# Performance work log

Hardware: AMD Instinct MI355X
Metric: run time of the kernel (lower is better)

Reference implementation:

```python
import jax, jax.numpy as jnp
import numpy as np
from jax import lax

D_MODEL = 768
N_LAYER = 4
D_STATE = 16
D_CONV = 4
EXPAND = 2
VOCAB = 32000
B = 1
L = 1024
D_INNER = D_MODEL * EXPAND
EPS = 1e-5


def setup_inputs() -> dict:
    key = jax.random.key(0)
    ks = jax.random.split(key, 8)
    s = 0.02
    A_row = jnp.log(jnp.arange(1, D_STATE + 1, dtype=jnp.float32))  # log(1..N)
    return {
        "idx": jax.random.randint(ks[0], (B, L), 0, VOCAB),
        "embed": jax.random.normal(ks[1], (VOCAB, D_MODEL), jnp.float32) * s,
        "norm_w": jnp.ones((N_LAYER, D_MODEL), jnp.float32),
        "W_in": jax.random.normal(ks[2], (N_LAYER, 2 * D_INNER, D_MODEL), jnp.float32) * s,
        "conv_w": jax.random.normal(ks[3], (N_LAYER, D_INNER, 1, D_CONV), jnp.float32) * s,
        "conv_b": jnp.zeros((N_LAYER, D_INNER), jnp.float32),
        "W_x": jax.random.normal(ks[4], (N_LAYER, 2 * D_STATE + 1, D_INNER), jnp.float32) * s,
        "dt_w": jax.random.normal(ks[5], (N_LAYER, D_INNER, 1), jnp.float32) * s,
        "dt_b": jnp.zeros((N_LAYER, D_INNER), jnp.float32),
        "A_log": jnp.tile(A_row, (N_LAYER, D_INNER, 1)),
        "Dp": jnp.ones((N_LAYER, D_INNER), jnp.float32),
        "out_w": jax.random.normal(ks[6], (N_LAYER, D_MODEL, D_INNER), jnp.float32) * s,
        "norm_f_w": jnp.ones((D_MODEL,), jnp.float32),
    }


def rmsnorm(x, w):
    return x / jnp.sqrt(jnp.mean(x * x, axis=-1, keepdims=True) + EPS) * w


def selective_scan(xc, W_x, dt_w, dt_b, A_log, Dp):
    # xc: [B, L, D_INNER]
    A = -jnp.exp(A_log)                               # [D, N]
    xp = xc @ W_x.T                                   # [B, L, 2N+1]
    dt_r = xp[..., :1]
    Bv = xp[..., 1:1 + D_STATE]                       # [B, L, N]
    Cv = xp[..., 1 + D_STATE:]                        # [B, L, N]
    dt = jax.nn.softplus(dt_r * dt_w[:, 0] + dt_b)    # [B, L, D]
    dA = jnp.exp(dt[..., None] * A)                   # [B, L, D, N]
    dBx = dt[..., None] * Bv[:, :, None, :] * xc[..., None]  # [B, L, D, N]

    def step(h, inp):
        dA_t, dBx_t, C_t = inp
        h = dA_t * h + dBx_t                          # [B, D, N]
        y = jnp.einsum('bdn,bn->bd', h, C_t)          # [B, D]
        return h, y

    h0 = jnp.zeros((xc.shape[0], D_INNER, D_STATE), xc.dtype)
    _, ys = lax.scan(step, h0, (dA.transpose(1, 0, 2, 3),
                                dBx.transpose(1, 0, 2, 3),
                                Cv.transpose(1, 0, 2)))
    return ys.transpose(1, 0, 2) + xc * Dp            # [B, L, D]


def mamba_block(x, W_in, conv_w, conv_b, W_x, dt_w, dt_b, A_log, Dp, out_w):
    xz = x @ W_in.T                                   # [B, L, 2*D_INNER]
    x_ssm, z = jnp.split(xz, 2, axis=-1)
    # depthwise causal conv1d (torch pads both sides then keeps first L == left pad only)
    xc = lax.conv_general_dilated(x_ssm.transpose(0, 2, 1), conv_w, (1,),
                                  [(D_CONV - 1, 0)],
                                  feature_group_count=D_INNER,
                                  dimension_numbers=('NCH', 'OIH', 'NCH'))
    xc = (xc + conv_b[None, :, None]).transpose(0, 2, 1)
    xc = jax.nn.silu(xc)
    y = selective_scan(xc, W_x, dt_w, dt_b, A_log, Dp)
    y = y * jax.nn.silu(z)
    return y @ out_w.T


def reference(idx, embed, norm_w, W_in, conv_w, conv_b, W_x, dt_w, dt_b, A_log, Dp, out_w, norm_f_w):
    x = embed[idx]  # dropout in eval mode == identity
    for i in range(N_LAYER):
        x = x + mamba_block(rmsnorm(x, norm_w[i]), W_in[i], conv_w[i], conv_b[i],
                            W_x[i], dt_w[i], dt_b[i], A_log[i], Dp[i], out_w[i])
    x = rmsnorm(x, norm_f_w)
    logits = x @ embed.T  # tied lm_head
    return logits
```

## Files before the change

### kernel.cpp

```cpp
#include <hip/hip_runtime.h>

#define D_MODEL 768
#define D_INNER 1536
#define D_XZ    3072
#define D_STATE 16
#define LSEQ    1024
#define NCHUNK  32
#define CLEN    32

typedef float  floatx4 __attribute__((ext_vector_type(4)));
typedef __bf16 bf16x2  __attribute__((ext_vector_type(2)));
typedef __bf16 bf16x8  __attribute__((ext_vector_type(8)));

__device__ __forceinline__ float softplus_f(float x) {
  float e = __expf(-fabsf(x));
  return fmaxf(x, 0.f) + __logf(1.f + e);
}
__device__ __forceinline__ float silu_f(float x) {
  return x / (1.f + __expf(-x));
}
__device__ __forceinline__ void gload_lds16(const void* g, void* l) {
  __builtin_amdgcn_global_load_lds(
      (const __attribute__((address_space(1))) void*)g,
      (__attribute__((address_space(3))) void*)l, 16, 0, 0);
}

template <int N> __device__ __forceinline__ void waitcnt_vm() {
  static_assert(N == 0 || N == 2 || N == 3 || N == 4, "unsupported vmcnt");
  if constexpr (N == 0) asm volatile("s_waitcnt vmcnt(0)" ::: "memory");
  else if constexpr (N == 2) asm volatile("s_waitcnt vmcnt(2)" ::: "memory");
  else if constexpr (N == 3) asm volatile("s_waitcnt vmcnt(3)" ::: "memory");
  else if constexpr (N == 4) asm volatile("s_waitcnt vmcnt(4)" ::: "memory");
}

__global__ __launch_bounds__(256) void k_cvt(const float* __restrict__ src,
                                             __bf16* __restrict__ dst) {
  size_t i = ((size_t)blockIdx.x * 256 + threadIdx.x) * 8;
  float4 a = *(const float4*)(src + i);
  float4 b = *(const float4*)(src + i + 4);
  bf16x8 o;
  o[0] = (__bf16)a.x; o[1] = (__bf16)a.y; o[2] = (__bf16)a.z; o[3] = (__bf16)a.w;
  o[4] = (__bf16)b.x; o[5] = (__bf16)b.y; o[6] = (__bf16)b.z; o[7] = (__bf16)b.w;
  *(bf16x8*)(dst + i) = o;
}

__global__ __launch_bounds__(256) void k_gather(const float* __restrict__ embed,
                                                const int* __restrict__ idx,
                                                float* __restrict__ x) {
  int t = blockIdx.x;
  int tok = idx[t];
  const float* src = embed + (size_t)tok * D_MODEL;
  float* dst = x + (size_t)t * D_MODEL;
  for (int c = threadIdx.x; c < D_MODEL; c += 256) dst[c] = src[c];
}

__global__ __launch_bounds__(256) void k_rmsnorm_bf(const float* __restrict__ x,
                                                    const float* __restrict__ w,
                                                    __bf16* __restrict__ o) {
  int lane = threadIdx.x & 63;
  int row = blockIdx.x * 4 + (threadIdx.x >> 6);
  const float* xr = x + (size_t)row * D_MODEL;
  float2 v[6];
  float ss = 0.f;
#pragma unroll
  for (int i = 0; i < 6; i++) {
    v[i] = *(const float2*)(xr + lane * 2 + i * 128);
    ss += v[i].x * v[i].x + v[i].y * v[i].y;
  }
#pragma unroll
  for (int m = 32; m; m >>= 1) ss += __shfl_xor(ss, m, 64);
  float r = rsqrtf(ss * (1.f / 768.f) + 1e-5f);
  __bf16* orow = o + (size_t)row * D_MODEL;
#pragma unroll
  for (int i = 0; i < 6; i++) {
    float2 wv = *(const float2*)(w + lane * 2 + i * 128);
    bf16x2 p;
    p[0] = (__bf16)(v[i].x * r * wv.x);
    p[1] = (__bf16)(v[i].y * r * wv.y);
    *(bf16x2*)(orow + lane * 2 + i * 128) = p;
  }
}

template <int TM, int TN>
__global__ __launch_bounds__(256) void k_gemm_bb(const __bf16* __restrict__ A,
                                                 const __bf16* __restrict__ B,
                                                 const float* res, float* __restrict__ C,
                                                 int M, int N, int K, int mTiles) {
  constexpr int MT  = TM / 32;
  constexpr int NTL = TN / 32;
  constexpr int NLA = TM / 64;
  constexpr int NLB = TN / 64;
  constexpr int NL  = NLA + NLB;
  __shared__ __attribute__((aligned(16))) __bf16 As[2][TM * 32];
  __shared__ __attribute__((aligned(16))) __bf16 Bs[2][TN * 32];
  const int tid = threadIdx.x;
  const int lane = tid & 63, wave = tid >> 6;
  const int fr = lane & 15, q = lane >> 4, kq = q * 8;

  int id = blockIdx.x;
  int per = gridDim.x >> 3;
  int v = (id & 7) * per + (id >> 3);
  int nt = v / mTiles, mt_ = v % mTiles;
  const int Mblk = mt_ * TM, Nblk = nt * TN;

  const int wm = (wave & 1) * (TM / 2), wn = (wave >> 1) * (TN / 2);

  const int row_s = tid >> 2;
  const int col_s = (tid & 3) * 8;
  const __bf16* Ag = A + (size_t)(Mblk + row_s) * K + col_s;
  const __bf16* Bg = B + (size_t)(Nblk + row_s) * K + col_s;

  floatx4 acc[MT][NTL];
#pragma unroll
  for (int i = 0; i < MT; i++)
#pragma unroll
    for (int j = 0; j < NTL; j++) {
      floatx4 z = {0.f, 0.f, 0.f, 0.f};
      acc[i][j] = z;
    }

  const int KT = K >> 5;

#pragma unroll
  for (int i = 0; i < NLA; i++)
    gload_lds16(Ag + (size_t)(64 * i) * K, &As[0][tid * 8 + i * 2048]);
#pragma unroll
  for (int i = 0; i < NLB; i++)
    gload_lds16(Bg + (size_t)(64 * i) * K, &Bs[0][tid * 8 + i * 2048]);

  for (int kt = 0; kt < KT; kt++) {
    const int cur = kt & 1;
    if (kt + 1 < KT) {
      const int k1 = (kt + 1) << 5;
#pragma unroll
      for (int i = 0; i < NLA; i++)
        gload_lds16(Ag + (size_t)(64 * i) * K + k1, &As[cur ^ 1][tid * 8 + i * 2048]);
#pragma unroll
      for (int i = 0; i < NLB; i++)
        gload_lds16(Bg + (size_t)(64 * i) * K + k1, &Bs[cur ^ 1][tid * 8 + i * 2048]);
      waitcnt_vm<NL>();
    } else {
      waitcnt_vm<0>();
    }
    __builtin_amdgcn_s_barrier();

    bf16x8 af[MT], bfr[NTL];
#pragma unroll
    for (int mt = 0; mt < MT; mt++)
      af[mt] = *(const bf16x8*)&As[cur][(wm + mt * 16 + fr) * 32 + kq];
#pragma unroll
    for (int ntl = 0; ntl < NTL; ntl++)
      bfr[ntl] = *(const bf16x8*)&Bs[cur][(wn + ntl * 16 + fr) * 32 + kq];
#pragma unroll
    for (int mt = 0; mt < MT; mt++)
#pragma unroll
      for (int ntl = 0; ntl < NTL; ntl++)
        acc[mt][ntl] = __builtin_amdgcn_mfma_f32_16x16x32_bf16(af[mt], bfr[ntl], acc[mt][ntl], 0, 0, 0);

    __builtin_amdgcn_s_barrier();
  }

#pragma unroll
  for (int mt = 0; mt < MT; mt++)
#pragma unroll
    for (int ntl = 0; ntl < NTL; ntl++) {
      int r = Mblk + wm + mt * 16 + q * 4;
      int c = Nblk + wn + ntl * 16 + fr;
#pragma unroll
      for (int i = 0; i < 4; i++) {
        size_t o = (size_t)(r + i) * N + c;
        float vv = acc[mt][ntl][i];
        if (res) vv += res[o];
        C[o] = vv;
      }
    }
}

__global__ __launch_bounds__(256) void k_xpconv(const float* __restrict__ xz,
                                                const float* __restrict__ cw4,
                                                const float* __restrict__ cb,
                                                const float* __restrict__ Wx,
                                                float* __restrict__ xc,
                                                float* __restrict__ xp) {
  __shared__ float red[4][33];
  int t = blockIdx.x;
  int wave = threadIdx.x >> 6, lane = threadIdx.x & 63;
  float acc[33];
#pragma unroll
  for (int j = 0; j < 33; j++) acc[j] = 0.f;
  for (int ii = 0; ii < 6; ii++) {
    int k = wave * 384 + ii * 64 + lane;
    float4 w = *(const float4*)(cw4 + (size_t)k * 4);
    float wv[4] = {w.x, w.y, w.z, w.w};
    float vv = cb[k];
#pragma unroll
    for (int jj = 0; jj < 4; jj++) {
      int ts = t - 3 + jj;
      if (ts >= 0) vv += wv[jj] * xz[(size_t)ts * D_XZ + k];
    }
    float xcv = silu_f(vv);
    xc[(size_t)t * D_INNER + k] = xcv;
#pragma unroll
    for (int j = 0; j < 33; j++) acc[j] += xcv * Wx[(size_t)j * D_INNER + k];
  }
#pragma unroll
  for (int j = 0; j < 33; j++) {
    float s = acc[j];
#pragma unroll
    for (int m = 32; m; m >>= 1) s += __shfl_xor(s, m, 64);
    if (lane == j) red[wave][j] = s;
  }
  __syncthreads();
  int j = threadIdx.x;
  if (j < 33) xp[(size_t)t * 33 + j] = red[0][j] + red[1][j] + red[2][j] + red[3][j];
}

__global__ __launch_bounds__(256) void k_scan1(const float* __restrict__ xp,
                                               const float* __restrict__ xc,
                                               const float* __restrict__ dtw,
                                               const float* __restrict__ dtb,
                                               const float* __restrict__ Alog,
                                               float* __restrict__ hend,
                                               float* __restrict__ Pp) {
  __shared__ float sxp[CLEN * 33];
  int c = blockIdx.x;
  int d = blockIdx.y * 256 + threadIdx.x;
  for (int i = threadIdx.x; i < CLEN * 33; i += 256) sxp[i] = xp[(size_t)c * CLEN * 33 + i];
  __syncthreads();
  float Av[16];
#pragma unroll
  for (int n = 0; n < 16; n++) Av[n] = -__expf(Alog[(size_t)d * 16 + n]);
  float w_ = dtw[d], b_ = dtb[d];
  float h[16], P[16];
#pragma unroll
  for (int n = 0; n < 16; n++) { h[n] = 0.f; P[n] = 1.f; }
  const float* xcc = xc + (size_t)(c * CLEN) * D_INNER + d;
  for (int tl = 0; tl < CLEN; tl++) {
    float dtr = sxp[tl * 33];
    float xv = xcc[(size_t)tl * D_INNER];
    float dt = softplus_f(dtr * w_ + b_);
    float sx = dt * xv;
#pragma unroll
    for (int n = 0; n < 16; n++) {
      float dA = __expf(dt * Av[n]);
      h[n] = dA * h[n] + sx * sxp[tl * 33 + 1 + n];
      P[n] *= dA;
    }
  }
  size_t o = ((size_t)c * D_INNER + d) * 16;
#pragma unroll
  for (int n = 0; n < 16; n++) { hend[o + n] = h[n]; Pp[o + n] = P[n]; }
}

__global__ __launch_bounds__(256) void k_scan2(const float* __restrict__ xp,
                                               const float* __restrict__ xc,
                                               const float* __restrict__ xz,
                                               const float* __restrict__ dtw,
                                               const float* __restrict__ dtb,
                                               const float* __restrict__ Alog,
                                               const float* __restrict__ Dp,
                                               const float* __restrict__ hend,
                                               const float* __restrict__ Pp,
                                               __bf16* __restrict__ g) {
  __shared__ float sxp[CLEN * 33];
  int c = blockIdx.x;
  int d = blockIdx.y * 256 + threadIdx.x;
  for (int i = threadIdx.x; i < CLEN * 33; i += 256) sxp[i] = xp[(size_t)c * CLEN * 33 + i];
  __syncthreads();
  float Av[16];
#pragma unroll
  for (int n = 0; n < 16; n++) Av[n] = -__expf(Alog[(size_t)d * 16 + n]);
  float w_ = dtw[d], b_ = dtb[d], Dv = Dp[d];
  float h[16];
#pragma unroll
  for (int n = 0; n < 16; n++) h[n] = 0.f;
  for (int c2 = 0; c2 < c; c2++) {
    size_t o = ((size_t)c2 * D_INNER + d) * 16;
#pragma unroll
    for (int n4 = 0; n4 < 4; n4++) {
      float4 hv = *(const float4*)(hend + o + n4 * 4);
      float4 pv = *(const float4*)(Pp + o + n4 * 4);
      h[n4 * 4 + 0] = pv.x * h[n4 * 4 + 0] + hv.x;
      h[n4 * 4 + 1] = pv.y * h[n4 * 4 + 1] + hv.y;
      h[n4 * 4 + 2] = pv.z * h[n4 * 4 + 2] + hv.z;
      h[n4 * 4 + 3] = pv.w * h[n4 * 4 + 3] + hv.w;
    }
  }
  for (int tl = 0; tl < CLEN; tl++) {
    int t = c * CLEN + tl;
    float dtr = sxp[tl * 33];
    float xv = xc[(size_t)t * D_INNER + d];
    float dt = softplus_f(dtr * w_ + b_);
    float sx = dt * xv;
    float y = 0.f;
#pragma unroll
    for (int n = 0; n < 16; n++) {
      float dA = __expf(dt * Av[n]);
      h[n] = dA * h[n] + sx * sxp[tl * 33 + 1 + n];
      y += h[n] * sxp[tl * 33 + 17 + n];
    }
    float z = xz[(size_t)t * D_XZ + D_INNER + d];
    g[(size_t)t * D_INNER + d] = (__bf16)((y + xv * Dv) * silu_f(z));
  }
}

extern "C" void kernel_launch(void* const* d_in, const int* in_sizes, int n_in,
                              void* d_out, int out_size, void* d_ws, size_t ws_size,
                              hipStream_t stream) {
  const int*   idx     = (const int*)d_in[0];
  const float* embed   = (const float*)d_in[1];
  const float* norm_w  = (const float*)d_in[2];
  const float* W_in    = (const float*)d_in[3];
  const float* conv_w  = (const float*)d_in[4];
  const float* conv_b  = (const float*)d_in[5];
  const float* W_x     = (const float*)d_in[6];
  const float* dt_w    = (const float*)d_in[7];
  const float* dt_b    = (const float*)d_in[8];
  const float* A_log   = (const float*)d_in[9];
  const float* Dp      = (const float*)d_in[10];
  const float* out_w   = (const float*)d_in[11];
  const float* norm_fw = (const float*)d_in[12];
  float* out = (float*)d_out;

  float*  x    = (float*)d_ws;
  __bf16* xnb  = (__bf16*)(x + 786432);
  float*  xp   = (float*)(xnb + 786432);
  float*  Pp   = xp + 33792;
  __bf16* gbf  = (__bf16*)(Pp + 786432);
  __bf16* pool = gbf + 1572864;
  __bf16* W_in_bf  = pool;
  __bf16* out_w_bf = pool + 9437184;
  float*  xz   = (float*)(out_w_bf + 4718592);
  float*  xc   = xz + 3145728;
  float*  hend = xc + 1572864;
  __bf16* emb_bf = pool;

  k_cvt<<<4608, 256, 0, stream>>>(W_in, W_in_bf);
  k_cvt<<<2304, 256, 0, stream>>>(out_w, out_w_bf);

  k_gather<<<1024, 256, 0, stream>>>(embed, idx, x);

  for (int l = 0; l < 4; l++) {
    k_rmsnorm_bf<<<256, 256, 0, stream>>>(x, norm_w + (size_t)l * D_MODEL, xnb);
    k_gemm_bb<64, 128><<<384, 256, 0, stream>>>(xnb, W_in_bf + (size_t)l * D_XZ * D_MODEL,
                                                nullptr, xz, 1024, D_XZ, D_MODEL, 16);
    k_xpconv<<<1024, 256, 0, stream>>>(xz, conv_w + (size_t)l * D_INNER * 4,
                                       conv_b + (size_t)l * D_INNER,
                                       W_x + (size_t)l * 33 * D_INNER, xc, xp);
    k_scan1<<<dim3(NCHUNK, 6), 256, 0, stream>>>(xp, xc, dt_w + (size_t)l * D_INNER,
                                                 dt_b + (size_t)l * D_INNER,
                                                 A_log + (size_t)l * D_INNER * 16, hend, Pp);
    k_scan2<<<dim3(NCHUNK, 6), 256, 0, stream>>>(xp, xc, xz, dt_w + (size_t)l * D_INNER,
                                                 dt_b + (size_t)l * D_INNER,
                                                 A_log + (size_t)l * D_INNER * 16,
                                                 Dp + (size_t)l * D_INNER, hend, Pp, gbf);
    k_gemm_bb<64, 64><<<192, 256, 0, stream>>>(gbf, out_w_bf + (size_t)l * D_MODEL * D_INNER,
                                               x, x, 1024, D_MODEL, D_INNER, 16);
  }

  k_cvt<<<12000, 256, 0, stream>>>(embed, emb_bf);
  k_rmsnorm_bf<<<256, 256, 0, stream>>>(x, norm_fw, xnb);
  k_gemm_bb<128, 128><<<2000, 256, 0, stream>>>(xnb, emb_bf, nullptr, out,
                                                1024, 32000, D_MODEL, 8);
}
```

Before: 865.1 us.

## Deepen GEMM LDS pipeline to four stages and XOR-swizzle LDS layout

```diff
diff --git a/kernel.cpp b/kernel.cpp
--- a/kernel.cpp
+++ b/kernel.cpp
@@ -26,12 +26,9 @@
 }
 
 template <int N> __device__ __forceinline__ void waitcnt_vm() {
-  static_assert(N == 0 || N == 2 || N == 3 || N == 4, "unsupported vmcnt");
-  if constexpr (N == 0) asm volatile("s_waitcnt vmcnt(0)" ::: "memory");
-  else if constexpr (N == 2) asm volatile("s_waitcnt vmcnt(2)" ::: "memory");
-  else if constexpr (N == 3) asm volatile("s_waitcnt vmcnt(3)" ::: "memory");
-  else if constexpr (N == 4) asm volatile("s_waitcnt vmcnt(4)" ::: "memory");
-}
+  asm volatile("s_waitcnt vmcnt(%0)" ::"n"(N) : "memory");
+}
+__device__ __forceinline__ void cfence() { asm volatile("" ::: "memory"); }
 
 __global__ __launch_bounds__(256) void k_cvt(const float* __restrict__ src,
                                              __bf16* __restrict__ dst) {
@@ -91,24 +88,23 @@
   constexpr int NLA = TM / 64;
   constexpr int NLB = TN / 64;
   constexpr int NL  = NLA + NLB;
-  __shared__ __attribute__((aligned(16))) __bf16 As[2][TM * 32];
-  __shared__ __attribute__((aligned(16))) __bf16 Bs[2][TN * 32];
+  __shared__ __attribute__((aligned(16))) __bf16 As[4][TM * 32];
+  __shared__ __attribute__((aligned(16))) __bf16 Bs[4][TN * 32];
   const int tid = threadIdx.x;
   const int lane = tid & 63, wave = tid >> 6;
-  const int fr = lane & 15, q = lane >> 4, kq = q * 8;
+  const int fr = lane & 15, q = lane >> 4;
 
   int id = blockIdx.x;
   int per = gridDim.x >> 3;
   int v = (id & 7) * per + (id >> 3);
   int nt = v / mTiles, mt_ = v % mTiles;
   const int Mblk = mt_ * TM, Nblk = nt * TN;
-
   const int wm = (wave & 1) * (TM / 2), wn = (wave >> 1) * (TN / 2);
 
   const int row_s = tid >> 2;
-  const int col_s = (tid & 3) * 8;
-  const __bf16* Ag = A + (size_t)(Mblk + row_s) * K + col_s;
-  const __bf16* Bg = B + (size_t)(Nblk + row_s) * K + col_s;
+  const int cs = ((tid & 3) ^ ((row_s >> 1) & 3)) * 8;
+  const __bf16* Ag = A + (size_t)(Mblk + row_s) * K + cs;
+  const __bf16* Bg = B + (size_t)(Nblk + row_s) * K + cs;
 
   floatx4 acc[MT][NTL];
 #pragma unroll
@@ -121,50 +117,63 @@
 
   const int KT = K >> 5;
 
-#pragma unroll
-  for (int i = 0; i < NLA; i++)
-    gload_lds16(Ag + (size_t)(64 * i) * K, &As[0][tid * 8 + i * 2048]);
-#pragma unroll
-  for (int i = 0; i < NLB; i++)
-    gload_lds16(Bg + (size_t)(64 * i) * K, &Bs[0][tid * 8 + i * 2048]);
-
-  for (int kt = 0; kt < KT; kt++) {
-    const int cur = kt & 1;
-    if (kt + 1 < KT) {
-      const int k1 = (kt + 1) << 5;
-#pragma unroll
-      for (int i = 0; i < NLA; i++)
-        gload_lds16(Ag + (size_t)(64 * i) * K + k1, &As[cur ^ 1][tid * 8 + i * 2048]);
-#pragma unroll
-      for (int i = 0; i < NLB; i++)
-        gload_lds16(Bg + (size_t)(64 * i) * K + k1, &Bs[cur ^ 1][tid * 8 + i * 2048]);
-      waitcnt_vm<NL>();
-    } else {
-      waitcnt_vm<0>();
-    }
-    __builtin_amdgcn_s_barrier();
-
-    bf16x8 af[MT], bfr[NTL];
-#pragma unroll
-    for (int mt = 0; mt < MT; mt++)
-      af[mt] = *(const bf16x8*)&As[cur][(wm + mt * 16 + fr) * 32 + kq];
-#pragma unroll
-    for (int ntl = 0; ntl < NTL; ntl++)
-      bfr[ntl] = *(const bf16x8*)&Bs[cur][(wn + ntl * 16 + fr) * 32 + kq];
-#pragma unroll
-    for (int mt = 0; mt < MT; mt++)
-#pragma unroll
-      for (int ntl = 0; ntl < NTL; ntl++)
-        acc[mt][ntl] = __builtin_amdgcn_mfma_f32_16x16x32_bf16(af[mt], bfr[ntl], acc[mt][ntl], 0, 0, 0);
-
-    __builtin_amdgcn_s_barrier();
-  }
+#define STAGE_T(t)                                                            \
+  do {                                                                        \
+    const int _b = (t) & 3;                                                   \
+    const int _k0 = (t) << 5;                                                 \
+    _Pragma("unroll") for (int i = 0; i < NLA; i++)                           \
+        gload_lds16(Ag + (size_t)(64 * i) * K + _k0,                          \
+                    &As[_b][tid * 8 + i * 2048]);                             \
+    _Pragma("unroll") for (int i = 0; i < NLB; i++)                           \
+        gload_lds16(Bg + (size_t)(64 * i) * K + _k0,                          \
+                    &Bs[_b][tid * 8 + i * 2048]);                             \
+  } while (0)
+
+#define STEP_T(kt, WN)                                                        \
+  do {                                                                        \
+    const int _cur = (kt) & 3;                                                \
+    waitcnt_vm<WN>();                                                         \
+    __builtin_amdgcn_s_barrier();          \
+    cfence();                                                                 \
+    bf16x8 af[MT], bfr[NTL];                                                  \
+    _Pragma("unroll") for (int mt = 0; mt < MT; mt++) {                       \
+      const int R = wm + mt * 16 + fr;                                        \
+      af[mt] = *(const bf16x8*)&As[_cur][R * 32 + ((q ^ ((R >> 1) & 3)) << 3)]; \
+    }                                                                         \
+    _Pragma("unroll") for (int ntl = 0; ntl < NTL; ntl++) {                   \
+      const int R = wn + ntl * 16 + fr;                                       \
+      bfr[ntl] = *(const bf16x8*)&Bs[_cur][R * 32 + ((q ^ ((R >> 1) & 3)) << 3)]; \
+    }                                                                         \
+    _Pragma("unroll") for (int mt = 0; mt < MT; mt++)                         \
+      _Pragma("unroll") for (int ntl = 0; ntl < NTL; ntl++)                   \
+        acc[mt][ntl] = __builtin_amdgcn_mfma_f32_16x16x32_bf16(               \
+            af[mt], bfr[ntl], acc[mt][ntl], 0, 0, 0);                         \
+    cfence();                                                                 \
+    __builtin_amdgcn_s_barrier();              \
+    cfence();                                                                 \
+  } while (0)
+
+  STAGE_T(0);
+  STAGE_T(1);
+  STAGE_T(2);
+
+  int kt = 0;
+  for (; kt < KT - 3; ++kt) {
+    STAGE_T(kt + 3);
+    STEP_T(kt, 3 * NL);
+  }
+  STEP_T(kt, 2 * NL); ++kt;
+  STEP_T(kt, 1 * NL); ++kt;
+  STEP_T(kt, 0);
+
+#undef STAGE_T
+#undef STEP_T
 
 #pragma unroll
   for (int mt = 0; mt < MT; mt++)
 #pragma unroll
     for (int ntl = 0; ntl < NTL; ntl++) {
-      int r = Mblk + wm + mt * 16 + q * 4;
+      int r = Mblk + wm + mt * 16 + (lane >> 4) * 4;
       int c = Nblk + wn + ntl * 16 + fr;
 #pragma unroll
       for (int i = 0; i < 4; i++) {
```

New measurement: 873.6 us. No clear change (+1.0%).
